# Kernel tuning notes

Measured on AMD Instinct MI355X. Metric: run time of the kernel, lower is better.

The kernel has to match this reference:

```python
import jax, jax.numpy as jnp
import numpy as np

N = 20000      # nodes
E = 320000     # directed edges (self-loops added inside reference)
DIN = 128      # input_dim
HID = 64       # hidden_dim
H = 4          # num_heads
B = 16         # graphs in batch
OUT = 1        # output_dim
NEG_SLOPE = 0.2


def setup_inputs() -> dict:
    key = jax.random.key(0)
    ks = jax.random.split(key, 20)
    p = lambda k, shape: (jax.random.normal(k, shape, jnp.float32) * 0.05)
    x = jax.random.normal(ks[0], (N, DIN), jnp.float32)
    edge_index = jax.random.randint(ks[1], (2, E), 0, N, dtype=jnp.int64)
    batch = jnp.sort(jax.random.randint(ks[2], (N,), 0, B, dtype=jnp.int64))
    return {
        "x": x, "edge_index": edge_index, "batch": batch,
        # gat1: DIN -> (H, HID), concat
        "W1": p(ks[3], (DIN, H * HID)), "as1": p(ks[4], (H, HID)), "ad1": p(ks[5], (H, HID)), "b1": jnp.zeros((H * HID,), jnp.float32),
        # gat2: H*HID -> (H, HID), concat
        "W2": p(ks[6], (H * HID, H * HID)), "as2": p(ks[7], (H, HID)), "ad2": p(ks[8], (H, HID)), "b2": jnp.zeros((H * HID,), jnp.float32),
        # gat_out: H*HID -> (1, HID), mean (concat=False)
        "W3": p(ks[9], (H * HID, HID)), "as3": p(ks[10], (1, HID)), "ad3": p(ks[11], (1, HID)), "b3": jnp.zeros((HID,), jnp.float32),
        "wp": p(ks[12], (HID, 1)), "bp": jnp.zeros((1,), jnp.float32),
        "wr": p(ks[13], (HID, OUT)), "br": jnp.zeros((OUT,), jnp.float32),
    }


def _gat_layer(x, W, a_src, a_dst, bias, src, dst, heads, concat):
    n = x.shape[0]
    h = (x @ W).reshape(n, heads, -1)                      # [N,H,C]
    e_src = (h * a_src).sum(-1)                            # [N,H]
    e_dst = (h * a_dst).sum(-1)                            # [N,H]
    e = jax.nn.leaky_relu(e_src[src] + e_dst[dst], NEG_SLOPE)  # [Etot,H]
    # segment softmax over destination node (self-loops guarantee non-empty)
    m = jax.ops.segment_max(e, dst, num_segments=n)
    e = jnp.exp(e - m[dst])
    den = jax.ops.segment_sum(e, dst, num_segments=n)
    alpha = e / den[dst]                                   # [Etot,H]
    out = jax.ops.segment_sum(h[src] * alpha[..., None], dst, num_segments=n)  # [N,H,C]
    out = out.reshape(n, -1) if concat else out.mean(axis=1)
    return out + bias


def reference(x, edge_index, batch, W1, as1, ad1, b1, W2, as2, ad2, b2,
              W3, as3, ad3, b3, wp, bp, wr, br):
    n = x.shape[0]
    loops = jnp.arange(n, dtype=edge_index.dtype)
    src = jnp.concatenate([edge_index[0], loops])
    dst = jnp.concatenate([edge_index[1], loops])

    h = jax.nn.elu(_gat_layer(x, W1, as1, ad1, b1, src, dst, H, True))
    h = jax.nn.elu(_gat_layer(h, W2, as2, ad2, b2, src, dst, H, True))
    h = jax.nn.elu(_gat_layer(h, W3, as3, ad3, b3, src, dst, 1, False))  # [N,HID]

    attn = jax.nn.sigmoid(h @ wp + bp)                     # [N,1]
    hw = h * attn                                          # [N,HID]
    sums = jax.ops.segment_sum(hw, batch, num_segments=B)  # [B,HID]
    counts = jax.ops.segment_sum(jnp.ones((n,), hw.dtype), batch, num_segments=B)
    pooled = sums / jnp.maximum(counts, 1.0)[:, None]
    return pooled @ wr + br                                # [B,OUT]
```

## Files before the change

kernel.cpp:

```cpp
#include <hip/hip_runtime.h>


typedef unsigned short u16;
typedef __attribute__((ext_vector_type(8))) short bf16x8;
typedef __attribute__((ext_vector_type(4))) float f32x4;

__device__ __forceinline__ u16 bf16rn(float x) {
    unsigned u = __float_as_uint(x);
    u += 0x7FFFu + ((u >> 16) & 1u);
    return (u16)(u >> 16);
}
__device__ __forceinline__ float bf16f(u16 h) {
    return __uint_as_float(((unsigned)h) << 16);
}

__device__ __forceinline__ void gload16(const u16* g, u16* l) {
    __builtin_amdgcn_global_load_lds(
        (const __attribute__((address_space(1))) unsigned int*)g,
        (__attribute__((address_space(3))) unsigned int*)l, 16, 0, 0);
}

__global__ void edge_hist_k(const int* __restrict__ ei, int E, int n, int* __restrict__ deg) {
    int i = blockIdx.x * blockDim.x + threadIdx.x;
    if (i >= E + n) return;
    int dst = (i < E) ? ei[E + i] : (i - E);
    atomicAdd(&deg[dst], 1);
}

__global__ __launch_bounds__(1024) void scan_excl_k(const int* __restrict__ deg, int* __restrict__ rowptr,
                                                    int* __restrict__ cursor, int n) {
    __shared__ int part[1024];
    int tid = threadIdx.x;
    int chunk = (n + 1023) / 1024;
    int lo = tid * chunk;
    int hi = lo + chunk;
    if (lo > n) lo = n;
    if (hi > n) hi = n;
    int s = 0;
    for (int i = lo; i < hi; ++i) s += deg[i];
    part[tid] = s;
    __syncthreads();
    for (int off = 1; off < 1024; off <<= 1) {
        int v = (tid >= off) ? part[tid - off] : 0;
        __syncthreads();
        part[tid] += v;
        __syncthreads();
    }
    int run = (tid == 0) ? 0 : part[tid - 1];
    for (int i = lo; i < hi; ++i) {
        rowptr[i] = run;
        cursor[i] = run;
        run += deg[i];
    }
    if (tid == 1023) rowptr[n] = run;
}

__global__ void edge_scatter_k(const int* __restrict__ ei, int E, int n,
                               int* __restrict__ cursor, int* __restrict__ srcs) {
    int i = blockIdx.x * blockDim.x + threadIdx.x;
    if (i >= E + n) return;
    int src, dst;
    if (i < E) { src = ei[i]; dst = ei[E + i]; }
    else       { src = i - E; dst = src; }
    int pos = atomicAdd(&cursor[dst], 1);
    srcs[pos] = src;
}

__global__ void split_bf16_k(const float* __restrict__ in, u16* __restrict__ hi,
                             u16* __restrict__ lo, int n4) {
    int i = blockIdx.x * 256 + threadIdx.x;
    if (i >= n4) return;
    float4 v = reinterpret_cast<const float4*>(in)[i];
    u16 hx = bf16rn(v.x), hy = bf16rn(v.y), hz = bf16rn(v.z), hw = bf16rn(v.w);
    ushort4 H = make_ushort4(hx, hy, hz, hw);
    ushort4 L = make_ushort4(bf16rn(v.x - bf16f(hx)), bf16rn(v.y - bf16f(hy)),
                             bf16rn(v.z - bf16f(hz)), bf16rn(v.w - bf16f(hw)));
    reinterpret_cast<ushort4*>(hi)[i] = H;
    reinterpret_cast<ushort4*>(lo)[i] = L;
}

__global__ void splitT_bf16_k(const float* __restrict__ W, u16* __restrict__ thi,
                              u16* __restrict__ tlo, int K, int Nn) {
    int idx = blockIdx.x * 256 + threadIdx.x;
    if (idx >= K * Nn) return;
    int k = idx / Nn, nn = idx - k * Nn;
    float v = W[idx];
    u16 h = bf16rn(v);
    u16 l = bf16rn(v - bf16f(h));
    thi[(size_t)nn * K + k] = h;
    tlo[(size_t)nn * K + k] = l;
}

template <int NF>
__global__ __launch_bounds__(256) void gemm_lds_k(
        const u16* __restrict__ Ahi, const u16* __restrict__ Alo,
        const u16* __restrict__ Bthi, const u16* __restrict__ Btlo,
        float* __restrict__ C, int M, int Nn, int K) {
    __shared__ u16 Ah[2][4][64 * 8];
    __shared__ u16 Al[2][4][64 * 8];
    const int mb = (M + 63) >> 6;
    const int mi = blockIdx.x % mb;
    const int ni = blockIdx.x / mb;
    const int m0 = mi * 64;
    const int n0 = ni * (NF * 64);
    const int wv = threadIdx.x >> 6;
    const int lane = threadIdx.x & 63;
    const int rr = lane & 15;
    const int kg = lane >> 4;

    int srow = m0 + lane; if (srow > M - 1) srow = M - 1;
    const u16* sh = Ahi + (size_t)srow * K + wv * 8;
    const u16* sl = Alo + (size_t)srow * K + wv * 8;

    const u16* pbh[NF];
    const u16* pbl[NF];
#pragma unroll
    for (int nf = 0; nf < NF; ++nf) {
        int col = n0 + (wv * NF + nf) * 16 + rr;
        pbh[nf] = Bthi + (size_t)col * K + kg * 8;
        pbl[nf] = Btlo + (size_t)col * K + kg * 8;
    }

    f32x4 acc[4][NF];
#pragma unroll
    for (int mf = 0; mf < 4; ++mf)
#pragma unroll
        for (int nf = 0; nf < NF; ++nf) acc[mf][nf] = (f32x4){0.f, 0.f, 0.f, 0.f};

    bf16x8 bhc[NF], blc[NF], bhn[NF], bln[NF];
#pragma unroll
    for (int nf = 0; nf < NF; ++nf) {
        bhc[nf] = *reinterpret_cast<const bf16x8*>(pbh[nf]);
        blc[nf] = *reinterpret_cast<const bf16x8*>(pbl[nf]);
    }
    gload16(sh, &Ah[0][wv][0]);
    gload16(sl, &Al[0][wv][0]);
    __syncthreads();

    const int NT = K >> 5;
    for (int t = 0; t < NT; ++t) {
        const int cur = t & 1;
        if (t + 1 < NT) {
            const int kc = (t + 1) << 5;
#pragma unroll
            for (int nf = 0; nf < NF; ++nf) {
                bhn[nf] = *reinterpret_cast<const bf16x8*>(pbh[nf] + kc);
                bln[nf] = *reinterpret_cast<const bf16x8*>(pbl[nf] + kc);
            }
            gload16(sh + kc, &Ah[cur ^ 1][wv][0]);
            gload16(sl + kc, &Al[cur ^ 1][wv][0]);
        }
        bf16x8 ah[4], al[4];
#pragma unroll
        for (int mf = 0; mf < 4; ++mf) {
            ah[mf] = *reinterpret_cast<const bf16x8*>(&Ah[cur][kg][(mf * 16 + rr) * 8]);
            al[mf] = *reinterpret_cast<const bf16x8*>(&Al[cur][kg][(mf * 16 + rr) * 8]);
        }
#pragma unroll
        for (int mf = 0; mf < 4; ++mf)
#pragma unroll
            for (int nf = 0; nf < NF; ++nf) {
                acc[mf][nf] = __builtin_amdgcn_mfma_f32_16x16x32_bf16(ah[mf], bhc[nf], acc[mf][nf], 0, 0, 0);
                acc[mf][nf] = __builtin_amdgcn_mfma_f32_16x16x32_bf16(ah[mf], blc[nf], acc[mf][nf], 0, 0, 0);
                acc[mf][nf] = __builtin_amdgcn_mfma_f32_16x16x32_bf16(al[mf], bhc[nf], acc[mf][nf], 0, 0, 0);
            }
#pragma unroll
        for (int nf = 0; nf < NF; ++nf) { bhc[nf] = bhn[nf]; blc[nf] = bln[nf]; }
        __syncthreads();
    }

#pragma unroll
    for (int mf = 0; mf < 4; ++mf)
#pragma unroll
        for (int nf = 0; nf < NF; ++nf)
#pragma unroll
            for (int rg = 0; rg < 4; ++rg) {
                int row = m0 + mf * 16 + kg * 4 + rg;
                if (row < M)
                    C[(size_t)row * Nn + n0 + (wv * NF + nf) * 16 + rr] = acc[mf][nf][rg];
            }
}

__global__ void attn_scores4_k(const float* __restrict__ hin, const float* __restrict__ a_src,
                               const float* __restrict__ a_dst, float* __restrict__ esrc,
                               float* __restrict__ edst, int n) {
    int node = blockIdx.x * 4 + (threadIdx.x >> 6);
    int lane = threadIdx.x & 63;
    if (node >= n) return;
    float4 hv  = *reinterpret_cast<const float4*>(&hin[(size_t)node * 256 + lane * 4]);
    float4 asv = *reinterpret_cast<const float4*>(&a_src[lane * 4]);
    float4 adv = *reinterpret_cast<const float4*>(&a_dst[lane * 4]);
    float vs = hv.x * asv.x + hv.y * asv.y + hv.z * asv.z + hv.w * asv.w;
    float vd = hv.x * adv.x + hv.y * adv.y + hv.z * adv.z + hv.w * adv.w;
#pragma unroll
    for (int off = 8; off; off >>= 1) {
        vs += __shfl_xor(vs, off);
        vd += __shfl_xor(vd, off);
    }
    if ((lane & 15) == 0) {
        int h = lane >> 4;
        esrc[node * 4 + h] = vs;
        edst[node * 4 + h] = vd;
    }
}

__global__ void attn_scores1_k(const float* __restrict__ hin, const float* __restrict__ a_src,
                               const float* __restrict__ a_dst, float* __restrict__ esrc,
                               float* __restrict__ edst, int n) {
    int node = blockIdx.x * 4 + (threadIdx.x >> 6);
    int lane = threadIdx.x & 63;
    if (node >= n) return;
    float hv = hin[(size_t)node * 64 + lane];
    float vs = hv * a_src[lane];
    float vd = hv * a_dst[lane];
#pragma unroll
    for (int off = 32; off; off >>= 1) {
        vs += __shfl_xor(vs, off);
        vd += __shfl_xor(vd, off);
    }
    if (lane == 0) { esrc[node] = vs; edst[node] = vd; }
}

__global__ __launch_bounds__(256) void gat_aggregate4_k(
        const float* __restrict__ hin, const float* __restrict__ esrc,
        const float* __restrict__ edst, const int* __restrict__ rowptr,
        const int* __restrict__ srcs, const float* __restrict__ bias,
        u16* __restrict__ ghi, u16* __restrict__ glo, int n) {
    int d = blockIdx.x * 4 + (threadIdx.x >> 6);
    int lane = threadIdx.x & 63;
    if (d >= n) return;
    const int hh = lane >> 4;
    const int jj = lane & 15;
    float ed = edst[d * 4 + hh];
    int lo = rowptr[d], hi = rowptr[d + 1];
    float4 acc = make_float4(0.f, 0.f, 0.f, 0.f);
    float den = 0.f;
    for (int base = lo; base < hi; base += 32) {
        int cnt = min(32, hi - base);
        int i0 = base + jj, i1 = base + 16 + jj;
        int s0 = srcs[(i0 < hi) ? i0 : lo];
        int s1 = srcs[(i1 < hi) ? i1 : lo];
        float e0 = esrc[s0 * 4 + hh] + ed;
        e0 = (e0 >= 0.f) ? e0 : 0.2f * e0;
        float w0 = (jj < cnt) ? __expf(e0) : 0.f;
        float e1 = esrc[s1 * 4 + hh] + ed;
        e1 = (e1 >= 0.f) ? e1 : 0.2f * e1;
        float w1 = (jj + 16 < cnt) ? __expf(e1) : 0.f;
        float ws = w0 + w1;
#pragma unroll
        for (int off = 1; off < 16; off <<= 1) ws += __shfl_xor(ws, off);
        den += ws;
        auto loadrow = [&](int j) -> float4 {
            j = (j < cnt) ? j : (cnt - 1);
            int sp = __shfl((j < 16) ? s0 : s1, j & 15);
            return *reinterpret_cast<const float4*>(&hin[(size_t)sp * 256 + lane * 4]);
        };
        auto wsel = [&](int j) -> float {
            return __shfl((j < 16) ? w0 : w1, (lane & 48) | (j & 15));
        };
        float4 p0 = loadrow(0), p1 = loadrow(1), p2 = loadrow(2), p3 = loadrow(3);
        for (int j = 0; j < cnt; j += 4) {
            float4 q0 = p0, q1 = p1, q2 = p2, q3 = p3;
            p0 = loadrow(j + 4);
            p1 = loadrow(j + 5);
            p2 = loadrow(j + 6);
            p3 = loadrow(j + 7);
            float wA = wsel(j), wB = wsel(j + 1), wC = wsel(j + 2), wD = wsel(j + 3);
            acc.x = fmaf(wA, q0.x, acc.x); acc.y = fmaf(wA, q0.y, acc.y);
            acc.z = fmaf(wA, q0.z, acc.z); acc.w = fmaf(wA, q0.w, acc.w);
            acc.x = fmaf(wB, q1.x, acc.x); acc.y = fmaf(wB, q1.y, acc.y);
            acc.z = fmaf(wB, q1.z, acc.z); acc.w = fmaf(wB, q1.w, acc.w);
            acc.x = fmaf(wC, q2.x, acc.x); acc.y = fmaf(wC, q2.y, acc.y);
            acc.z = fmaf(wC, q2.z, acc.z); acc.w = fmaf(wC, q2.w, acc.w);
            acc.x = fmaf(wD, q3.x, acc.x); acc.y = fmaf(wD, q3.y, acc.y);
            acc.z = fmaf(wD, q3.z, acc.z); acc.w = fmaf(wD, q3.w, acc.w);
        }
    }
    float inv = 1.f / den;
    float4 bv = *reinterpret_cast<const float4*>(&bias[lane * 4]);
    float4 o;
    o.x = acc.x * inv + bv.x;
    o.y = acc.y * inv + bv.y;
    o.z = acc.z * inv + bv.z;
    o.w = acc.w * inv + bv.w;
    o.x = (o.x > 0.f) ? o.x : expm1f(o.x);
    o.y = (o.y > 0.f) ? o.y : expm1f(o.y);
    o.z = (o.z > 0.f) ? o.z : expm1f(o.z);
    o.w = (o.w > 0.f) ? o.w : expm1f(o.w);
    u16 hx = bf16rn(o.x), hy = bf16rn(o.y), hz = bf16rn(o.z), hw = bf16rn(o.w);
    ushort4 H = make_ushort4(hx, hy, hz, hw);
    ushort4 L = make_ushort4(bf16rn(o.x - bf16f(hx)), bf16rn(o.y - bf16f(hy)),
                             bf16rn(o.z - bf16f(hz)), bf16rn(o.w - bf16f(hw)));
    *reinterpret_cast<ushort4*>(&ghi[(size_t)d * 256 + lane * 4]) = H;
    *reinterpret_cast<ushort4*>(&glo[(size_t)d * 256 + lane * 4]) = L;
}

__global__ __launch_bounds__(256) void gat_aggregate1_attn_k(
        const float* __restrict__ hin, const float* __restrict__ esrc,
        const float* __restrict__ edst, const int* __restrict__ rowptr,
        const int* __restrict__ srcs, const float* __restrict__ bias,
        const float* __restrict__ wp, const float* __restrict__ bp,
        float* __restrict__ gout, float* __restrict__ attn, int n) {
    int d = blockIdx.x * 4 + (threadIdx.x >> 6);
    int lane = threadIdx.x & 63;
    if (d >= n) return;
    float ed = edst[d];
    int lo = rowptr[d], hi = rowptr[d + 1];
    float den = 0.f, acc = 0.f;
    for (int base = lo; base < hi; base += 64) {
        int cnt = min(64, hi - base);
        int idx = base + lane;
        int s = srcs[(idx < hi) ? idx : lo];
        float e = esrc[s] + ed;
        e = (e >= 0.f) ? e : 0.2f * e;
        float w = (lane < cnt) ? __expf(e) : 0.f;
        float ws = w;
#pragma unroll
        for (int off = 1; off < 64; off <<= 1) ws += __shfl_xor(ws, off);
        den += ws;
        auto loadrow = [&](int j) -> float {
            j = (j < cnt) ? j : (cnt - 1);
            int sp = __shfl(s, j);
            return hin[(size_t)sp * 64 + lane];
        };
        float p0 = loadrow(0), p1 = loadrow(1), p2 = loadrow(2), p3 = loadrow(3);
        for (int j = 0; j < cnt; j += 4) {
            float q0 = p0, q1 = p1, q2 = p2, q3 = p3;
            p0 = loadrow(j + 4);
            p1 = loadrow(j + 5);
            p2 = loadrow(j + 6);
            p3 = loadrow(j + 7);
            acc = fmaf(__shfl(w, j), q0, acc);
            acc = fmaf(__shfl(w, j + 1), q1, acc);
            acc = fmaf(__shfl(w, j + 2), q2, acc);
            acc = fmaf(__shfl(w, j + 3), q3, acc);
        }
    }
    float o = acc / den + bias[lane];
    o = (o > 0.f) ? o : expm1f(o);
    gout[(size_t)d * 64 + lane] = o;
    float v = o * wp[lane];
#pragma unroll
    for (int off = 32; off; off >>= 1) v += __shfl_xor(v, off);
    if (lane == 0) attn[d] = 1.f / (1.f + __expf(-(v + bp[0])));
}

__global__ void pool_partial_k(const float* __restrict__ g3, const float* __restrict__ attn,
                               const int* __restrict__ batch, int n, float* __restrict__ sums) {
    int wid = blockIdx.x * (blockDim.x >> 6) + (threadIdx.x >> 6);
    int lane = threadIdx.x & 63;
    int nwaves = gridDim.x * (blockDim.x >> 6);
    int per = (n + nwaves - 1) / nwaves;
    int i0 = wid * per;
    int i1 = i0 + per;
    if (i1 > n) i1 = n;
    if (i0 >= i1) return;
    int cur = batch[i0];
    float acc = 0.f;
    for (int i = i0; i < i1; ++i) {
        int b = batch[i];
        if (b != cur) {
            atomicAdd(&sums[cur * 64 + lane], acc);
            acc = 0.f;
            cur = b;
        }
        acc += g3[(size_t)i * 64 + lane] * attn[i];
    }
    atomicAdd(&sums[cur * 64 + lane], acc);
}

__global__ void regress_k(const float* __restrict__ sums, const int* __restrict__ batch, int n,
                          const float* __restrict__ wr, const float* __restrict__ br,
                          float* __restrict__ out, int B) {
    int b = threadIdx.x >> 6;
    int lane = threadIdx.x & 63;
    if (b >= B) return;
    int lo = 0, hi = n;
    while (lo < hi) { int mid = (lo + hi) >> 1; if (batch[mid] < b) lo = mid + 1; else hi = mid; }
    int seg_lo = lo;
    lo = 0; hi = n;
    while (lo < hi) { int mid = (lo + hi) >> 1; if (batch[mid] < b + 1) lo = mid + 1; else hi = mid; }
    float cnt = (float)(lo - seg_lo);
    if (cnt < 1.f) cnt = 1.f;
    float v = (sums[b * 64 + lane] / cnt) * wr[lane];
#pragma unroll
    for (int off = 32; off; off >>= 1) v += __shfl_xor(v, off);
    if (lane == 0) out[b] = v + br[0];
}

extern "C" void kernel_launch(void* const* d_in, const int* in_sizes, int n_in,
                              void* d_out, int out_size, void* d_ws, size_t ws_size,
                              hipStream_t stream) {
    const float* x   = (const float*)d_in[0];
    const int*   ei  = (const int*)d_in[1];
    const int*   bat = (const int*)d_in[2];
    const float* W1  = (const float*)d_in[3];
    const float* as1 = (const float*)d_in[4];
    const float* ad1 = (const float*)d_in[5];
    const float* b1  = (const float*)d_in[6];
    const float* W2  = (const float*)d_in[7];
    const float* as2 = (const float*)d_in[8];
    const float* ad2 = (const float*)d_in[9];
    const float* b2  = (const float*)d_in[10];
    const float* W3  = (const float*)d_in[11];
    const float* as3 = (const float*)d_in[12];
    const float* ad3 = (const float*)d_in[13];
    const float* b3  = (const float*)d_in[14];
    const float* wp  = (const float*)d_in[15];
    const float* bp  = (const float*)d_in[16];
    const float* wr  = (const float*)d_in[17];
    const float* br  = (const float*)d_in[18];
    float* out = (float*)d_out;

    const int N    = in_sizes[2];
    const int E    = in_sizes[1] / 2;
    const int DIN  = in_sizes[0] / N;
    const int Etot = E + N;
    const int Bc   = out_size;

    char* ws = (char*)d_ws;
    size_t off = 0;
    auto alloc = [&](size_t bytes) {
        void* p = ws + off;
        off = (off + bytes + 255) & ~(size_t)255;
        return p;
    };
    int*   deg    = (int*)alloc((size_t)N * 4);
    int*   rowptr = (int*)alloc((size_t)(N + 1) * 4);
    int*   cursor = (int*)alloc((size_t)N * 4);
    int*   srcs   = (int*)alloc((size_t)Etot * 4);
    float* bufA   = (float*)alloc((size_t)N * 256 * 4);
    u16*   Ahi    = (u16*)alloc((size_t)N * 256 * 2);
    u16*   Alo    = (u16*)alloc((size_t)N * 256 * 2);
    float* h3     = (float*)alloc((size_t)N * 64 * 4);
    float* g3     = (float*)alloc((size_t)N * 64 * 4);
    float* esrc   = (float*)alloc((size_t)N * 4 * 4);
    float* edst   = (float*)alloc((size_t)N * 4 * 4);
    float* attn   = (float*)alloc((size_t)N * 4);
    float* sums   = (float*)alloc((size_t)Bc * 64 * 4);
    u16*   w1hi   = (u16*)alloc((size_t)256 * DIN * 2);
    u16*   w1lo   = (u16*)alloc((size_t)256 * DIN * 2);
    u16*   w2hi   = (u16*)alloc((size_t)256 * 256 * 2);
    u16*   w2lo   = (u16*)alloc((size_t)256 * 256 * 2);
    u16*   w3hi   = (u16*)alloc((size_t)64 * 256 * 2);
    u16*   w3lo   = (u16*)alloc((size_t)64 * 256 * 2);
    (void)ws_size;

    hipMemsetAsync(deg, 0, (size_t)N * 4, stream);
    int eb = (Etot + 255) / 256;
    edge_hist_k<<<eb, 256, 0, stream>>>(ei, E, N, deg);
    scan_excl_k<<<1, 1024, 0, stream>>>(deg, rowptr, cursor, N);
    edge_scatter_k<<<eb, 256, 0, stream>>>(ei, E, N, cursor, srcs);

    splitT_bf16_k<<<(DIN * 256 + 255) / 256, 256, 0, stream>>>(W1, w1hi, w1lo, DIN, 256);
    splitT_bf16_k<<<(256 * 256 + 255) / 256, 256, 0, stream>>>(W2, w2hi, w2lo, 256, 256);
    splitT_bf16_k<<<(256 * 64 + 255) / 256, 256, 0, stream>>>(W3, w3hi, w3lo, 256, 64);
    split_bf16_k<<<(N * DIN / 4 + 255) / 256, 256, 0, stream>>>(x, Ahi, Alo, N * DIN / 4);

    const int mb = (N + 63) / 64;
    int nb4 = (N + 3) / 4;

    gemm_lds_k<2><<<mb * 2, 256, 0, stream>>>(Ahi, Alo, w1hi, w1lo, bufA, N, 256, DIN);
    attn_scores4_k<<<nb4, 256, 0, stream>>>(bufA, as1, ad1, esrc, edst, N);
    gat_aggregate4_k<<<nb4, 256, 0, stream>>>(bufA, esrc, edst, rowptr, srcs, b1, Ahi, Alo, N);

    gemm_lds_k<2><<<mb * 2, 256, 0, stream>>>(Ahi, Alo, w2hi, w2lo, bufA, N, 256, 256);
    attn_scores4_k<<<nb4, 256, 0, stream>>>(bufA, as2, ad2, esrc, edst, N);
    gat_aggregate4_k<<<nb4, 256, 0, stream>>>(bufA, esrc, edst, rowptr, srcs, b2, Ahi, Alo, N);

    gemm_lds_k<1><<<mb, 256, 0, stream>>>(Ahi, Alo, w3hi, w3lo, h3, N, 64, 256);
    attn_scores1_k<<<nb4, 256, 0, stream>>>(h3, as3, ad3, esrc, edst, N);
    gat_aggregate1_attn_k<<<nb4, 256, 0, stream>>>(h3, esrc, edst, rowptr, srcs, b3, wp, bp, g3, attn, N);

    hipMemsetAsync(sums, 0, (size_t)Bc * 64 * 4, stream);
    pool_partial_k<<<256, 256, 0, stream>>>(g3, attn, bat, N, sums);
    regress_k<<<1, 1024, 0, stream>>>(sums, bat, N, wr, br, out, Bc);
}
```

Baseline: 281.5 us.

## Fuse attention score computation into GEMM epilogue and deepen aggregate prefetch

Computes the per-node source/destination attention scores inside the GEMM epilogue from the accumulator registers, reducing across lanes and waves through shared memory. This removes the separate attn_scores kernels and their full re-read of the hidden features. Separately, the gather loops in both aggregate kernels now prefetch 8 neighbour rows instead of 4, which raises memory-level parallelism at the cost of more registers. The epilogue adds a barrier and reuses the A-tile shared buffer after the main loop.

Result: no change. 277.3 us (-1.5%).

```diff
diff --git a/kernel.cpp b/kernel.cpp
--- a/kernel.cpp
+++ b/kernel.cpp
@@ -95,7 +95,10 @@
 __global__ __launch_bounds__(256) void gemm_lds_k(
         const u16* __restrict__ Ahi, const u16* __restrict__ Alo,
         const u16* __restrict__ Bthi, const u16* __restrict__ Btlo,
-        float* __restrict__ C, int M, int Nn, int K) {
+        float* __restrict__ C,
+        const float* __restrict__ a_src, const float* __restrict__ a_dst,
+        float* __restrict__ esrc, float* __restrict__ edst,
+        int M, int Nn, int K) {
     __shared__ u16 Ah[2][4][64 * 8];
     __shared__ u16 Al[2][4][64 * 8];
     const int mb = (M + 63) >> 6;
@@ -103,8 +106,9 @@
     const int ni = blockIdx.x / mb;
     const int m0 = mi * 64;
     const int n0 = ni * (NF * 64);
-    const int wv = threadIdx.x >> 6;
-    const int lane = threadIdx.x & 63;
+    const int tid = threadIdx.x;
+    const int wv = tid >> 6;
+    const int lane = tid & 63;
     const int rr = lane & 15;
     const int kg = lane >> 4;
 
@@ -179,46 +183,65 @@
                 if (row < M)
                     C[(size_t)row * Nn + n0 + (wv * NF + nf) * 16 + rr] = acc[mf][nf][rg];
             }
-}
-
-__global__ void attn_scores4_k(const float* __restrict__ hin, const float* __restrict__ a_src,
-                               const float* __restrict__ a_dst, float* __restrict__ esrc,
-                               float* __restrict__ edst, int n) {
-    int node = blockIdx.x * 4 + (threadIdx.x >> 6);
-    int lane = threadIdx.x & 63;
-    if (node >= n) return;
-    float4 hv  = *reinterpret_cast<const float4*>(&hin[(size_t)node * 256 + lane * 4]);
-    float4 asv = *reinterpret_cast<const float4*>(&a_src[lane * 4]);
-    float4 adv = *reinterpret_cast<const float4*>(&a_dst[lane * 4]);
-    float vs = hv.x * asv.x + hv.y * asv.y + hv.z * asv.z + hv.w * asv.w;
-    float vd = hv.x * adv.x + hv.y * adv.y + hv.z * adv.z + hv.w * adv.w;
-#pragma unroll
-    for (int off = 8; off; off >>= 1) {
-        vs += __shfl_xor(vs, off);
-        vd += __shfl_xor(vd, off);
-    }
-    if ((lane & 15) == 0) {
-        int h = lane >> 4;
-        esrc[node * 4 + h] = vs;
-        edst[node * 4 + h] = vd;
-    }
-}
-
-__global__ void attn_scores1_k(const float* __restrict__ hin, const float* __restrict__ a_src,
-                               const float* __restrict__ a_dst, float* __restrict__ esrc,
-                               float* __restrict__ edst, int n) {
-    int node = blockIdx.x * 4 + (threadIdx.x >> 6);
-    int lane = threadIdx.x & 63;
-    if (node >= n) return;
-    float hv = hin[(size_t)node * 64 + lane];
-    float vs = hv * a_src[lane];
-    float vd = hv * a_dst[lane];
-#pragma unroll
-    for (int off = 32; off; off >>= 1) {
-        vs += __shfl_xor(vs, off);
-        vd += __shfl_xor(vd, off);
-    }
-    if (lane == 0) { esrc[node] = vs; edst[node] = vd; }
+
+    float asv[NF], adv[NF];
+#pragma unroll
+    for (int nf = 0; nf < NF; ++nf) {
+        int col = n0 + (wv * NF + nf) * 16 + rr;
+        asv[nf] = a_src[col];
+        adv[nf] = a_dst[col];
+    }
+    float ps[4][4], pd[4][4];
+#pragma unroll
+    for (int mf = 0; mf < 4; ++mf)
+#pragma unroll
+        for (int rg = 0; rg < 4; ++rg) {
+            float s = 0.f, dvv = 0.f;
+#pragma unroll
+            for (int nf = 0; nf < NF; ++nf) {
+                s = fmaf(acc[mf][nf][rg], asv[nf], s);
+                dvv = fmaf(acc[mf][nf][rg], adv[nf], dvv);
+            }
+#pragma unroll
+            for (int off = 1; off < 16; off <<= 1) {
+                s += __shfl_xor(s, off);
+                dvv += __shfl_xor(dvv, off);
+            }
+            ps[mf][rg] = s;
+            pd[mf][rg] = dvv;
+        }
+    float* sm_src = (float*)&Ah[0][0][0];
+    float* sm_dst = sm_src + 256;
+    if (rr == 0) {
+#pragma unroll
+        for (int mf = 0; mf < 4; ++mf)
+#pragma unroll
+            for (int rg = 0; rg < 4; ++rg) {
+                int rl = mf * 16 + kg * 4 + rg;
+                sm_src[wv * 64 + rl] = ps[mf][rg];
+                sm_dst[wv * 64 + rl] = pd[mf][rg];
+            }
+    }
+    __syncthreads();
+    if (tid < 64) {
+        int row = m0 + tid;
+        if (row < M) {
+            const int HTOT = Nn >> 6;
+            constexpr int WPH = 4 / NF;
+#pragma unroll
+            for (int hl = 0; hl < NF; ++hl) {
+                float es = 0.f, edv = 0.f;
+#pragma unroll
+                for (int w = 0; w < WPH; ++w) {
+                    es += sm_src[(hl * WPH + w) * 64 + tid];
+                    edv += sm_dst[(hl * WPH + w) * 64 + tid];
+                }
+                int hg = ni * NF + hl;
+                esrc[(size_t)row * HTOT + hg] = es;
+                edst[(size_t)row * HTOT + hg] = edv;
+            }
+        }
+    }
 }
 
 __global__ __launch_bounds__(256) void gat_aggregate4_k(
@@ -259,13 +282,16 @@
             return __shfl((j < 16) ? w0 : w1, (lane & 48) | (j & 15));
         };
         float4 p0 = loadrow(0), p1 = loadrow(1), p2 = loadrow(2), p3 = loadrow(3);
-        for (int j = 0; j < cnt; j += 4) {
+        float4 p4 = loadrow(4), p5 = loadrow(5), p6 = loadrow(6), p7 = loadrow(7);
+        for (int j = 0; j < cnt; j += 8) {
             float4 q0 = p0, q1 = p1, q2 = p2, q3 = p3;
-            p0 = loadrow(j + 4);
-            p1 = loadrow(j + 5);
-            p2 = loadrow(j + 6);
-            p3 = loadrow(j + 7);
-            float wA = wsel(j), wB = wsel(j + 1), wC = wsel(j + 2), wD = wsel(j + 3);
+            float4 q4 = p4, q5 = p5, q6 = p6, q7 = p7;
+            p0 = loadrow(j + 8);  p1 = loadrow(j + 9);
+            p2 = loadrow(j + 10); p3 = loadrow(j + 11);
+            p4 = loadrow(j + 12); p5 = loadrow(j + 13);
+            p6 = loadrow(j + 14); p7 = loadrow(j + 15);
+            float wA = wsel(j),     wB = wsel(j + 1), wC = wsel(j + 2), wD = wsel(j + 3);
+            float wE = wsel(j + 4), wF = wsel(j + 5), wG = wsel(j + 6), wH = wsel(j + 7);
             acc.x = fmaf(wA, q0.x, acc.x); acc.y = fmaf(wA, q0.y, acc.y);
             acc.z = fmaf(wA, q0.z, acc.z); acc.w = fmaf(wA, q0.w, acc.w);
             acc.x = fmaf(wB, q1.x, acc.x); acc.y = fmaf(wB, q1.y, acc.y);
@@ -274,6 +300,14 @@
             acc.z = fmaf(wC, q2.z, acc.z); acc.w = fmaf(wC, q2.w, acc.w);
             acc.x = fmaf(wD, q3.x, acc.x); acc.y = fmaf(wD, q3.y, acc.y);
             acc.z = fmaf(wD, q3.z, acc.z); acc.w = fmaf(wD, q3.w, acc.w);
+            acc.x = fmaf(wE, q4.x, acc.x); acc.y = fmaf(wE, q4.y, acc.y);
+            acc.z = fmaf(wE, q4.z, acc.z); acc.w = fmaf(wE, q4.w, acc.w);
+            acc.x = fmaf(wF, q5.x, acc.x); acc.y = fmaf(wF, q5.y, acc.y);
+            acc.z = fmaf(wF, q5.z, acc.z); acc.w = fmaf(wF, q5.w, acc.w);
+            acc.x = fmaf(wG, q6.x, acc.x); acc.y = fmaf(wG, q6.y, acc.y);
+            acc.z = fmaf(wG, q6.z, acc.z); acc.w = fmaf(wG, q6.w, acc.w);
+            acc.x = fmaf(wH, q7.x, acc.x); acc.y = fmaf(wH, q7.y, acc.y);
+            acc.z = fmaf(wH, q7.z, acc.z); acc.w = fmaf(wH, q7.w, acc.w);
         }
     }
     float inv = 1.f / den;
@@ -324,16 +358,22 @@
             return hin[(size_t)sp * 64 + lane];
         };
         float p0 = loadrow(0), p1 = loadrow(1), p2 = loadrow(2), p3 = loadrow(3);
-        for (int j = 0; j < cnt; j += 4) {
+        float p4 = loadrow(4), p5 = loadrow(5), p6 = loadrow(6), p7 = loadrow(7);
+        for (int j = 0; j < cnt; j += 8) {
             float q0 = p0, q1 = p1, q2 = p2, q3 = p3;
-            p0 = loadrow(j + 4);
-            p1 = loadrow(j + 5);
-            p2 = loadrow(j + 6);
-            p3 = loadrow(j + 7);
+            float q4 = p4, q5 = p5, q6 = p6, q7 = p7;
+            p0 = loadrow(j + 8);  p1 = loadrow(j + 9);
+            p2 = loadrow(j + 10); p3 = loadrow(j + 11);
+            p4 = loadrow(j + 12); p5 = loadrow(j + 13);
+            p6 = loadrow(j + 14); p7 = loadrow(j + 15);
             acc = fmaf(__shfl(w, j), q0, acc);
             acc = fmaf(__shfl(w, j + 1), q1, acc);
             acc = fmaf(__shfl(w, j + 2), q2, acc);
             acc = fmaf(__shfl(w, j + 3), q3, acc);
+            acc = fmaf(__shfl(w, j + 4), q4, acc);
+            acc = fmaf(__shfl(w, j + 5), q5, acc);
+            acc = fmaf(__shfl(w, j + 6), q6, acc);
+            acc = fmaf(__shfl(w, j + 7), q7, acc);
         }
     }
     float o = acc / den + bias[lane];
@@ -460,16 +500,13 @@
     const int mb = (N + 63) / 64;
     int nb4 = (N + 3) / 4;
 
-    gemm_lds_k<2><<<mb * 2, 256, 0, stream>>>(Ahi, Alo, w1hi, w1lo, bufA, N, 256, DIN);
-    attn_scores4_k<<<nb4, 256, 0, stream>>>(bufA, as1, ad1, esrc, edst, N);
+    gemm_lds_k<2><<<mb * 2, 256, 0, stream>>>(Ahi, Alo, w1hi, w1lo, bufA, as1, ad1, esrc, edst, N, 256, DIN);
     gat_aggregate4_k<<<nb4, 256, 0, stream>>>(bufA, esrc, edst, rowptr, srcs, b1, Ahi, Alo, N);
 
-    gemm_lds_k<2><<<mb * 2, 256, 0, stream>>>(Ahi, Alo, w2hi, w2lo, bufA, N, 256, 256);
-    attn_scores4_k<<<nb4, 256, 0, stream>>>(bufA, as2, ad2, esrc, edst, N);
+    gemm_lds_k<2><<<mb * 2, 256, 0, stream>>>(Ahi, Alo, w2hi, w2lo, bufA, as2, ad2, esrc, edst, N, 256, 256);
     gat_aggregate4_k<<<nb4, 256, 0, stream>>>(bufA, esrc, edst, rowptr, srcs, b2, Ahi, Alo, N);
 
-    gemm_lds_k<1><<<mb, 256, 0, stream>>>(Ahi, Alo, w3hi, w3lo, h3, N, 64, 256);
-    attn_scores1_k<<<nb4, 256, 0, stream>>>(h3, as3, ad3, esrc, edst, N);
+    gemm_lds_k<1><<<mb, 256, 0, stream>>>(Ahi, Alo, w3hi, w3lo, h3, as3, ad3, esrc, edst, N, 64, 256);
     gat_aggregate1_attn_k<<<nb4, 256, 0, stream>>>(h3, esrc, edst, rowptr, srcs, b3, wp, bp, g3, attn, N);
 
     hipMemsetAsync(sums, 0, (size_t)Bc * 64 * 4, stream);
```
